# Kernel tuning notes

Hardware: AMD Instinct MI355X
Metric: run time of the kernel (lower is better)

## Reference

```python
import jax, jax.numpy as jnp
import numpy as np
import math

B, T, C = 1, 2048, 2048
NH, HS = 16, 128          # hs = C // nh
NLQ, NLKV, DHR = 1536, 512, 64


def _rope(x, cos, sin):
    # x: [B, T, H, D]; cos/sin: [T, D//2]. Rotates pairs (even, odd) like
    # torch's complex-multiply apply_rotary_emb.
    xr = x.reshape(x.shape[:-1] + (-1, 2))
    x_re, x_im = xr[..., 0], xr[..., 1]
    c = cos[None, :, None, :]
    s = sin[None, :, None, :]
    out = jnp.stack([x_re * c - x_im * s, x_re * s + x_im * c], axis=-1)
    return out.reshape(x.shape)


def setup_inputs() -> dict:
    key = jax.random.key(0)
    ks = jax.random.split(key, 9)
    sc = 0.02  # init scale so logits stay sane
    x = jax.random.normal(ks[0], (B, T, C), jnp.float32)
    # RoPE tables (theta = 10000), matching precompute_freqs_cis
    inv = 1.0 / (10000.0 ** (jnp.arange(0, DHR, 2, dtype=jnp.float32) / DHR))
    ang = jnp.outer(jnp.arange(T, dtype=jnp.float32), inv)  # [T, DHR//2]
    return {
        "x": x,
        "freqs_cos": jnp.cos(ang),
        "freqs_sin": jnp.sin(ang),
        "W_dq": jax.random.normal(ks[1], (NLQ, C), jnp.float32) * sc,
        "W_uq": jax.random.normal(ks[2], (C, NLQ), jnp.float32) * sc,
        "W_dkv": jax.random.normal(ks[3], (NLKV, C), jnp.float32) * sc,
        "W_uk": jax.random.normal(ks[4], (C, NLKV), jnp.float32) * sc,
        "W_uv": jax.random.normal(ks[5], (C, NLKV), jnp.float32) * sc,
        "W_qr": jax.random.normal(ks[6], (NH * DHR, NLQ), jnp.float32) * sc,
        "W_kr": jax.random.normal(ks[7], (DHR, C), jnp.float32) * sc,
        "W_o": jax.random.normal(ks[8], (C, C), jnp.float32) * sc,
    }


def reference(x, freqs_cos, freqs_sin, W_dq, W_uq, W_dkv, W_uk, W_uv, W_qr, W_kr, W_o):
    # ---- low-rank query/kv down-projections ----
    c_q = x @ W_dq.T                       # [B,T,NLQ]
    c_kv = x @ W_dkv.T                     # [B,T,NLKV]  (no kv_cache: c_kv = new_c_kv)

    # ---- weight absorption (training path) ----
    # torch: W_uq.weight.view(1,nlq,nh,hs).transpose(1,2) @ W_uk.weight.view(1,nh,hs,nlkv)
    Wuq_h = W_uq.reshape(NLQ, NH, HS).transpose(1, 0, 2)   # [NH,NLQ,HS]
    Wuk_h = W_uk.reshape(NH, HS, NLKV)                     # [NH,HS,NLKV]
    k_eff = jnp.einsum('hql,hlk->hqk', Wuq_h, Wuk_h)       # [NH,NLQ,NLKV]
    # torch: (W_uv.weight.T @ W_o.weight.T).view(nlkv,nh,hs).transpose(0,1)
    v_eff = (W_uv.T @ W_o.T).reshape(NLKV, NH, HS).transpose(1, 0, 2)  # [NH,NLKV,HS]

    # ---- content attention scores in latent space ----
    attn_c = jnp.einsum('bhtk,bsk->bhts',
                        jnp.einsum('btq,hqk->bhtk', c_q, k_eff), c_kv)  # [B,NH,T,T]

    # ---- decoupled RoPE subspace ----
    k_r = _rope((x @ W_kr.T)[:, :, None, :], freqs_cos, freqs_sin)[:, :, 0, :]   # [B,T,DHR]
    q_r = _rope((c_q @ W_qr.T).reshape(B, T, NH, DHR), freqs_cos, freqs_sin)
    q_r = q_r.transpose(0, 2, 1, 3)                                              # [B,NH,T,DHR]
    attn_r = jnp.einsum('bhtd,bsd->bhts', q_r, k_r)                              # [B,NH,T,T]

    # ---- combine, causal mask, softmax ----
    scale = 1.0 / math.sqrt(HS + DHR)
    scores = (attn_c + attn_r) * scale
    causal = jnp.tril(jnp.ones((T, T), dtype=bool))  # mask = triu(diag=1) complement
    scores = jnp.where(causal[None, None], scores, jnp.float32(-jnp.inf))
    attn = jax.nn.softmax(scores, axis=-1)           # dropout p=0.0

    # ---- value path: attend in latent space, then absorbed up+output proj ----
    y_lat = jnp.einsum('bhts,bsk->bhtk', attn, c_kv)          # [B,NH,T,NLKV]
    y = jnp.einsum('bhtk,hkd->bhtd', y_lat, v_eff)            # [B,NH,T,HS]
    y = y.transpose(0, 2, 1, 3).reshape(B, T, C)              # [B,T,C] (W_o absorbed)
    return y
```

## Files before the change

kernel.cpp:

```cpp
#include <hip/hip_runtime.h>
#include <hip/hip_bf16.h>
#include <math.h>

typedef __bf16 bf16_t;
typedef __bf16 bf16x4 __attribute__((ext_vector_type(4)));
typedef __bf16 bf16x8 __attribute__((ext_vector_type(8)));
typedef float f32x4 __attribute__((ext_vector_type(4)));

#define T_DIM 2048
#define C_DIM 2048
#define NH 16
#define HS 128
#define NLQ 1536
#define NLKV 512
#define DHR 64
#define QKD 192

__device__ __forceinline__ int probe_f32(const bf16_t* __restrict__ x) {
  int lane = threadIdx.x & 63;
  int bad = 0;
#pragma unroll
  for (int i = 0; i < 4; ++i) {
    float v = (float)x[lane + i * 64];
    if (!(fabsf(v) < 1.0e6f)) bad = 1;
  }
  return (__ballot(bad) != 0ull) ? 1 : 0;
}

struct PrepPack {
  const void* src[9];
  bf16_t* dst[9];
  int n[9];
  const void* tsrc[2];
  bf16_t* tdst[2];
  int tR[2], tC[2], tbx[2];
};

__global__ __launch_bounds__(256) void prep_k(PrepPack p, const bf16_t* __restrict__ xprobe) {
  __shared__ bf16_t tile[32][33];
  const int f32 = probe_f32(xprobe);
  const int which = blockIdx.y;
  if (which < 9) {
    const int n = p.n[which];
    const int stride = gridDim.x * 256 * 8;
    for (int i = (blockIdx.x * 256 + threadIdx.x) * 8; i < n; i += stride) {
      if (f32) {
        const float* s = (const float*)p.src[which] + i;
        f32x4 lo = *(const f32x4*)s;
        f32x4 hi = *(const f32x4*)(s + 4);
        bf16x8 v;
#pragma unroll
        for (int j = 0; j < 4; ++j) { v[j] = (bf16_t)lo[j]; v[j + 4] = (bf16_t)hi[j]; }
        *(bf16x8*)(p.dst[which] + i) = v;
      } else {
        *(bf16x8*)(p.dst[which] + i) = *(const bf16x8*)((const bf16_t*)p.src[which] + i);
      }
    }
  } else {
    const int ts = which - 9;
    const int R = p.tR[ts], C = p.tC[ts], tbx = p.tbx[ts];
    const int ntiles = tbx * (R / 32);
    if ((int)blockIdx.x >= ntiles) return;
    const void* in = p.tsrc[ts];
    bf16_t* out = p.tdst[ts];
    int bx = (blockIdx.x % tbx) * 32, by = (blockIdx.x / tbx) * 32;
    int tx = threadIdx.x & 31, ty = threadIdx.x >> 5;
    for (int i = ty; i < 32; i += 8) {
      int r = by + i, c = bx + tx;
      size_t idx = (size_t)r * C + c;
      tile[i][tx] = f32 ? (bf16_t)((const float*)in)[idx] : ((const bf16_t*)in)[idx];
    }
    __syncthreads();
    for (int i = ty; i < 32; i += 8) {
      int r = bx + i, c = by + tx;
      out[(size_t)r * R + c] = tile[tx][i];
    }
  }
}

__device__ __forceinline__ void async16(const bf16_t* g, bf16_t* l) {
  __builtin_amdgcn_global_load_lds(
      (const __attribute__((address_space(1))) void*)g,
      (__attribute__((address_space(3))) void*)l, 16, 0, 0);
}

#define BM 128
#define BN 128
#define BKG 64

struct GDesc {
  const bf16_t* A; const bf16_t* B; bf16_t* C;
  int M, N, K, lda, ldb, ldc, mb, bx0;
};
struct GGrp { GDesc d[3]; };

__global__ __launch_bounds__(256) void gemm_group(GGrp g, int nseg) {
  int bx = blockIdx.x;
  int s = 0;
  while (s + 1 < nseg && bx >= g.d[s + 1].bx0) ++s;
  const GDesc D = g.d[s];
  const int local = bx - D.bx0;
  const int bm = (local % D.mb) * BM, bn = (local / D.mb) * BN;

  __shared__ bf16_t As[2][BM * BKG];
  __shared__ bf16_t Bs[2][BN * BKG];
  const int tid = threadIdx.x;
  const int lane = tid & 63;
  const int wave = tid >> 6;
  const int l16 = lane & 15, quad = lane >> 4;
  const int wm = (wave >> 1) * 64, wn = (wave & 1) * 64;
  f32x4 acc[4][4] = {};

  const int nt = D.K / BKG;

#pragma unroll
  for (int r = 0; r < 4; ++r) {
    int c = r * 256 + tid;
    int row = c >> 3;
    int c8 = (c & 7) ^ (row & 7);
    int ar = bm + row; if (ar > D.M - 1) ar = D.M - 1;
    int br = bn + row; if (br > D.N - 1) br = D.N - 1;
    async16(D.A + (size_t)ar * D.lda + c8 * 8, &As[0][c * 8]);
    async16(D.B + (size_t)br * D.ldb + c8 * 8, &Bs[0][c * 8]);
  }
  asm volatile("s_waitcnt vmcnt(0)" ::: "memory");
  __builtin_amdgcn_s_barrier();

  for (int t = 0; t < nt; ++t) {
    const int cur = t & 1;
    if (t + 1 < nt) {
      const int k0 = (t + 1) * BKG;
#pragma unroll
      for (int r = 0; r < 4; ++r) {
        int c = r * 256 + tid;
        int row = c >> 3;
        int c8 = (c & 7) ^ (row & 7);
        int ar = bm + row; if (ar > D.M - 1) ar = D.M - 1;
        int br = bn + row; if (br > D.N - 1) br = D.N - 1;
        async16(D.A + (size_t)ar * D.lda + k0 + c8 * 8, &As[cur ^ 1][c * 8]);
        async16(D.B + (size_t)br * D.ldb + k0 + c8 * 8, &Bs[cur ^ 1][c * 8]);
      }
    }
#pragma unroll
    for (int kk = 0; kk < 2; ++kk) {
      bf16x8 af[4], bfr[4];
#pragma unroll
      for (int i = 0; i < 4; ++i) {
        int row = wm + i * 16 + l16;
        af[i] = *(const bf16x8*)(&As[cur][row * BKG + (((kk * 4 + quad) ^ (row & 7)) * 8)]);
      }
#pragma unroll
      for (int j = 0; j < 4; ++j) {
        int row = wn + j * 16 + l16;
        bfr[j] = *(const bf16x8*)(&Bs[cur][row * BKG + (((kk * 4 + quad) ^ (row & 7)) * 8)]);
      }
#pragma unroll
      for (int i = 0; i < 4; ++i)
#pragma unroll
        for (int j = 0; j < 4; ++j)
          acc[i][j] = __builtin_amdgcn_mfma_f32_16x16x32_bf16(af[i], bfr[j], acc[i][j], 0, 0, 0);
    }
    asm volatile("s_waitcnt vmcnt(0)" ::: "memory");
    __builtin_amdgcn_s_barrier();
  }

#pragma unroll
  for (int i = 0; i < 4; ++i)
#pragma unroll
    for (int j = 0; j < 4; ++j)
#pragma unroll
      for (int r = 0; r < 4; ++r) {
        int gm = bm + wm + i * 16 + quad * 4 + r;
        int gn = bn + wn + j * 16 + l16;
        if (gm < D.M && gn < D.N) D.C[(size_t)gm * D.ldc + gn] = (bf16_t)acc[i][j][r];
      }
}

__global__ void pack_qk_k(const bf16_t* __restrict__ qcat, const bf16_t* __restrict__ khead,
                          const bf16_t* __restrict__ xa,
                          const bf16_t* __restrict__ fc, const bf16_t* __restrict__ fs,
                          bf16_t* __restrict__ Qp, bf16_t* __restrict__ Kp) {
  int idx = blockIdx.x * blockDim.x + threadIdx.x;
  if (idx >= NH * T_DIM * 96) return;
  int j = idx % 96;
  int t = (idx / 96) % T_DIM;
  int h = idx / (96 * T_DIM);
  if (blockIdx.y == 0) {
    const float scale = 0.07216878364870323f;
    bf16_t* out = Qp + ((size_t)h * T_DIM + t) * QKD;
    if (j < 64) {
      float a = (float)qcat[(size_t)t * 3072 + h * HS + 2 * j];
      float b = (float)qcat[(size_t)t * 3072 + h * HS + 2 * j + 1];
      out[2 * j] = (bf16_t)(a * scale);
      out[2 * j + 1] = (bf16_t)(b * scale);
    } else {
      int i = j - 64;
      float re = (float)qcat[(size_t)t * 3072 + 2048 + h * DHR + 2 * i];
      float im = (float)qcat[(size_t)t * 3072 + 2048 + h * DHR + 2 * i + 1];
      float c = (float)fc[t * 32 + i], s = (float)fs[t * 32 + i];
      out[HS + 2 * i] = (bf16_t)((re * c - im * s) * scale);
      out[HS + 2 * i + 1] = (bf16_t)((re * s + im * c) * scale);
    }
  } else {
    bf16_t* out = Kp + ((size_t)h * T_DIM + t) * QKD;
    if (j < 64) {
      out[2 * j] = khead[(size_t)t * C_DIM + h * HS + 2 * j];
      out[2 * j + 1] = khead[(size_t)t * C_DIM + h * HS + 2 * j + 1];
    } else {
      int i = j - 64;
      float re = (float)xa[(size_t)t * 2112 + 2048 + 2 * i];
      float im = (float)xa[(size_t)t * 2112 + 2048 + 2 * i + 1];
      float c = (float)fc[t * 32 + i], s = (float)fs[t * 32 + i];
      out[HS + 2 * i] = (bf16_t)(re * c - im * s);
      out[HS + 2 * i + 1] = (bf16_t)(re * s + im * c);
    }
  }
}

#define FBM 128
#define FBN 64
#define KPITCH 200
#define VPITCH 72
#define PPITCH 72

__global__ __launch_bounds__(256) void flash_k(const bf16_t* __restrict__ Qp,
                                               const bf16_t* __restrict__ Kp,
                                               const bf16_t* __restrict__ VT,
                                               void* __restrict__ Y,
                                               const bf16_t* __restrict__ xprobe,
                                               float* __restrict__ Opart,
                                               float* __restrict__ Mpart,
                                               float* __restrict__ Lpart) {
  __shared__ bf16_t Ksm[FBN * KPITCH];
  __shared__ bf16_t Vtsm[HS * VPITCH];
  __shared__ bf16_t Psm[4][32 * PPITCH];
  const int tid = threadIdx.x;
  const int lane = tid & 63, wave = tid >> 6;
  const int l16 = lane & 15, quad = lane >> 4;
  const int id = blockIdx.x;
  const int xcd = id & 7, slot = id >> 3;
  const int h = xcd + 8 * (slot / 24);
  const int p = slot % 24;
  int qt, kt0, kt1, partial;
  if (p < 16) {
    qt = 8 + (p >> 1);
    int half = qt + 1;
    kt0 = (p & 1) ? half : 0;
    kt1 = (p & 1) ? (2 * qt + 2) : half;
    partial = 1;
  } else {
    qt = 23 - p; kt0 = 0; kt1 = 2 * qt + 2; partial = 0;
  }
  const int qb = qt * FBM;
  const int f32out = probe_f32(xprobe);

  bf16x8 aq[2][6];
#pragma unroll
  for (int tt = 0; tt < 2; ++tt) {
    const bf16_t* qbase = Qp + ((size_t)h * T_DIM + qb + wave * 32 + tt * 16 + l16) * QKD;
#pragma unroll
    for (int c = 0; c < 6; ++c) aq[tt][c] = *(const bf16x8*)(qbase + c * 32 + quad * 8);
  }

  f32x4 o[2][8] = {};
  float m_i[2] = {-3.0e38f, -3.0e38f}, l_i[2] = {0.f, 0.f};

  const bf16_t* kg_base = Kp + (size_t)h * T_DIM * QKD;
  const bf16_t* vg_base = VT + (size_t)(h * HS) * T_DIM;

  bf16x8 kreg[6], vreg[4];
  {
    const bf16_t* kg = kg_base + (size_t)kt0 * FBN * QKD;
#pragma unroll
    for (int i = 0; i < 6; ++i) {
      int idx = i * 256 + tid;
      kreg[i] = *(const bf16x8*)(kg + (size_t)idx * 8);
    }
    const bf16_t* vg = vg_base + kt0 * FBN;
#pragma unroll
    for (int i = 0; i < 4; ++i) {
      int idx = i * 256 + tid, row = idx >> 3, c8 = idx & 7;
      vreg[i] = *(const bf16x8*)(vg + (size_t)row * T_DIM + c8 * 8);
    }
  }

  for (int kt = kt0; kt < kt1; ++kt) {
    __syncthreads();
#pragma unroll
    for (int i = 0; i < 6; ++i) {
      int idx = i * 256 + tid, row = idx / 24, c8 = idx % 24;
      *(bf16x8*)(Ksm + row * KPITCH + c8 * 8) = kreg[i];
    }
#pragma unroll
    for (int i = 0; i < 4; ++i) {
      int idx = i * 256 + tid, row = idx >> 3, c8 = idx & 7;
      *(bf16x8*)(Vtsm + row * VPITCH + c8 * 8) = vreg[i];
    }
    __syncthreads();
    if (kt + 1 < kt1) {
      const bf16_t* kg = kg_base + (size_t)(kt + 1) * FBN * QKD;
#pragma unroll
      for (int i = 0; i < 6; ++i) {
        int idx = i * 256 + tid;
        kreg[i] = *(const bf16x8*)(kg + (size_t)idx * 8);
      }
      const bf16_t* vg = vg_base + (kt + 1) * FBN;
#pragma unroll
      for (int i = 0; i < 4; ++i) {
        int idx = i * 256 + tid, row = idx >> 3, c8 = idx & 7;
        vreg[i] = *(const bf16x8*)(vg + (size_t)row * T_DIM + c8 * 8);
      }
    }
    f32x4 sc[2][4] = {};
#pragma unroll
    for (int nt = 0; nt < 4; ++nt)
#pragma unroll
      for (int c = 0; c < 6; ++c) {
        bf16x8 bk = *(const bf16x8*)(Ksm + (nt * 16 + l16) * KPITCH + c * 32 + quad * 8);
        sc[0][nt] = __builtin_amdgcn_mfma_f32_16x16x32_bf16(bk, aq[0][c], sc[0][nt], 0, 0, 0);
        sc[1][nt] = __builtin_amdgcn_mfma_f32_16x16x32_bf16(bk, aq[1][c], sc[1][nt], 0, 0, 0);
      }
    if (kt >= 2 * qt) {
#pragma unroll
      for (int tt = 0; tt < 2; ++tt) {
        int t_glob = qb + wave * 32 + tt * 16 + l16;
#pragma unroll
        for (int nt = 0; nt < 4; ++nt) {
          int s_base = kt * FBN + nt * 16 + quad * 4;
#pragma unroll
          for (int r = 0; r < 4; ++r)
            if (s_base + r > t_glob) sc[tt][nt][r] = -3.0e38f;
        }
      }
    }
#pragma unroll
    for (int tt = 0; tt < 2; ++tt) {
      float mx = sc[tt][0][0];
#pragma unroll
      for (int nt = 0; nt < 4; ++nt)
#pragma unroll
        for (int r = 0; r < 4; ++r) mx = fmaxf(mx, sc[tt][nt][r]);
      mx = fmaxf(mx, __shfl_xor(mx, 16, 64));
      mx = fmaxf(mx, __shfl_xor(mx, 32, 64));
      float mn = fmaxf(m_i[tt], mx);
      float alpha = exp2f((m_i[tt] - mn) * 1.4426950408889634f);
      float rs = 0.f;
#pragma unroll
      for (int nt = 0; nt < 4; ++nt) {
        bf16x4 pk;
#pragma unroll
        for (int r = 0; r < 4; ++r) {
          float pv = exp2f((sc[tt][nt][r] - mn) * 1.4426950408889634f);
          rs += pv;
          pk[r] = (bf16_t)pv;
        }
        *(bf16x4*)(&Psm[wave][(tt * 16 + l16) * PPITCH + nt * 16 + quad * 4]) = pk;
      }
      rs += __shfl_xor(rs, 16, 64);
      rs += __shfl_xor(rs, 32, 64);
      l_i[tt] = l_i[tt] * alpha + rs;
      m_i[tt] = mn;
#pragma unroll
      for (int dt = 0; dt < 8; ++dt) o[tt][dt] *= alpha;
    }
#pragma unroll
    for (int s2 = 0; s2 < 2; ++s2) {
      bf16x8 ap0 = *(const bf16x8*)(&Psm[wave][l16 * PPITCH + s2 * 32 + quad * 8]);
      bf16x8 ap1 = *(const bf16x8*)(&Psm[wave][(16 + l16) * PPITCH + s2 * 32 + quad * 8]);
#pragma unroll
      for (int dt = 0; dt < 8; ++dt) {
        bf16x8 bv = *(const bf16x8*)(Vtsm + (dt * 16 + l16) * VPITCH + s2 * 32 + quad * 8);
        o[0][dt] = __builtin_amdgcn_mfma_f32_16x16x32_bf16(bv, ap0, o[0][dt], 0, 0, 0);
        o[1][dt] = __builtin_amdgcn_mfma_f32_16x16x32_bf16(bv, ap1, o[1][dt], 0, 0, 0);
      }
    }
  }

  if (!partial) {
#pragma unroll
    for (int tt = 0; tt < 2; ++tt) {
      float inv = 1.0f / l_i[tt];
      int t = qb + wave * 32 + tt * 16 + l16;
#pragma unroll
      for (int dt = 0; dt < 8; ++dt) {
        size_t oi = (size_t)t * C_DIM + h * HS + dt * 16 + quad * 4;
        if (f32out) {
          f32x4 v;
#pragma unroll
          for (int r = 0; r < 4; ++r) v[r] = o[tt][dt][r] * inv;
          *(f32x4*)((float*)Y + oi) = v;
        } else {
          bf16x4 v;
#pragma unroll
          for (int r = 0; r < 4; ++r) v[r] = (bf16_t)(o[tt][dt][r] * inv);
          *(bf16x4*)((bf16_t*)Y + oi) = v;
        }
      }
    }
  } else {
    const int pi = h * 16 + p;
#pragma unroll
    for (int tt = 0; tt < 2; ++tt) {
      int rowl = wave * 32 + tt * 16 + l16;
      float* ob = Opart + ((size_t)pi * 128 + rowl) * 128;
#pragma unroll
      for (int dt = 0; dt < 8; ++dt) {
        f32x4 v = o[tt][dt];
        *(f32x4*)(ob + dt * 16 + quad * 4) = v;
      }
      if (quad == 0) {
        Mpart[(size_t)pi * 128 + rowl] = m_i[tt];
        Lpart[(size_t)pi * 128 + rowl] = l_i[tt];
      }
    }
  }
}

__global__ __launch_bounds__(256) void combine_k(const float* __restrict__ Opart,
                                                 const float* __restrict__ Mpart,
                                                 const float* __restrict__ Lpart,
                                                 void* __restrict__ Y,
                                                 const bf16_t* __restrict__ xprobe) {
  const int h = blockIdx.y;
  const int qi = blockIdx.x;
  const int pi0 = h * 16 + qi * 2, pi1 = pi0 + 1;
  const int row = threadIdx.x >> 1;
  const int c0 = (threadIdx.x & 1) * 64;
  const int f32out = probe_f32(xprobe);
  float m0 = Mpart[(size_t)pi0 * 128 + row], m1 = Mpart[(size_t)pi1 * 128 + row];
  float l0 = Lpart[(size_t)pi0 * 128 + row], l1 = Lpart[(size_t)pi1 * 128 + row];
  float ms = fmaxf(m0, m1);
  float w0 = exp2f((m0 - ms) * 1.4426950408889634f);
  float w1 = exp2f((m1 - ms) * 1.4426950408889634f);
  float inv = 1.0f / (l0 * w0 + l1 * w1);
  const float* O0 = Opart + ((size_t)pi0 * 128 + row) * 128 + c0;
  const float* O1 = Opart + ((size_t)pi1 * 128 + row) * 128 + c0;
  int t = (8 + qi) * 128 + row;
  size_t ob = (size_t)t * C_DIM + h * HS + c0;
#pragma unroll
  for (int d4 = 0; d4 < 64; d4 += 4) {
    f32x4 a = *(const f32x4*)(O0 + d4);
    f32x4 b = *(const f32x4*)(O1 + d4);
#pragma unroll
    for (int j = 0; j < 4; ++j) {
      float v = (a[j] * w0 + b[j] * w1) * inv;
      if (f32out) ((float*)Y)[ob + d4 + j] = v;
      else        ((bf16_t*)Y)[ob + d4 + j] = (bf16_t)v;
    }
  }
}

extern "C" void kernel_launch(void* const* d_in, const int* in_sizes, int n_in,
                              void* d_out, int out_size, void* d_ws, size_t ws_size,
                              hipStream_t stream) {
  bf16_t* w = (bf16_t*)d_ws;
  const bf16_t* xprobe = (const bf16_t*)d_in[0];

  if (ws_size < (size_t)34472000 * 2 + 128) return;

  bf16_t* fcc    = w + 64;
  bf16_t* fsc    = w + 65600;
  bf16_t* xc     = w + 131136;
  bf16_t* BigB   = w + 4325440;
  bf16_t* dqc    = BigB;
  bf16_t* dkvc   = BigB + 3145728;
  bf16_t* krc    = BigB + 4194304;
  bf16_t* Bq     = w + 8650816;
  bf16_t* W_uq_t = Bq;
  bf16_t* qrc    = Bq + 3145728;
  bf16_t* xa     = w + 13369408;
  bf16_t* qcat   = w + 17694784;
  bf16_t* k_head = w + 23986240;
  bf16_t* vhatT  = w + 28180544;
  bf16_t* ukc    = w + 32374848;
  bf16_t* Pt     = w + 33423424;
  bf16_t* woc    = qcat;
  bf16_t* W_uv_t = k_head;
  bf16_t* Qpack  = xc;
  bf16_t* Kpack  = qcat;
  float* Opart = (float*)(w + 6422592);
  float* Mpart = (float*)(w + 14811200);
  float* Lpart = (float*)(w + 14876736);

  PrepPack pp;
  const void* srcs[9] = {d_in[1], d_in[2], d_in[0], d_in[3], d_in[5], d_in[9], d_in[8], d_in[6], d_in[10]};
  bf16_t* dsts[9]     = {fcc,     fsc,     xc,      dqc,     dkvc,    krc,     qrc,     ukc,     woc};
  int ns[9] = {T_DIM * 32, T_DIM * 32, T_DIM * C_DIM, NLQ * C_DIM, NLKV * C_DIM,
               DHR * C_DIM, NH * DHR * NLQ, C_DIM * NLKV, C_DIM * C_DIM};
  for (int i = 0; i < 9; ++i) { pp.src[i] = srcs[i]; pp.dst[i] = dsts[i]; pp.n[i] = ns[i]; }
  pp.tsrc[0] = d_in[4]; pp.tdst[0] = W_uq_t; pp.tR[0] = 1536; pp.tC[0] = 2048; pp.tbx[0] = 64;
  pp.tsrc[1] = d_in[7]; pp.tdst[1] = W_uv_t; pp.tR[1] = 2048; pp.tC[1] = 512;  pp.tbx[1] = 16;
  prep_k<<<dim3(3072, 11), 256, 0, stream>>>(pp, xprobe);

  {
    GGrp g;
    g.d[0] = {xc,  BigB,   xa, 2048, 2112, 2048, 2048, 2048, 2112, 16, 0};
    g.d[1] = {woc, W_uv_t, Pt, 2048,  512, 2048, 2048, 2048,  512, 16, 272};
    gemm_group<<<336, 256, 0, stream>>>(g, 2);
  }
  {
    GGrp g;
    g.d[0] = {xa,        Bq,        qcat,   2048, 3072, 1536, 2112, 1536, 3072, 16, 0};
    g.d[1] = {xa + 1536, ukc,       k_head, 2048, 2048,  512, 2112,  512, 2048, 16, 384};
    g.d[2] = {Pt,        xa + 1536, vhatT,  2048, 2048,  512,  512, 2112, 2048, 16, 640};
    gemm_group<<<896, 256, 0, stream>>>(g, 3);
  }

  int pk = (NH * T_DIM * 96 + 255) / 256;
  pack_qk_k<<<dim3(pk, 2), 256, 0, stream>>>(qcat, k_head, xa, fcc, fsc, Qpack, Kpack);

  flash_k<<<dim3(384), 256, 0, stream>>>(Qpack, Kpack, vhatT, d_out, xprobe, Opart, Mpart, Lpart);
  combine_k<<<dim3(8, NH), 256, 0, stream>>>(Opart, Mpart, Lpart, d_out, xprobe);
}
```

Measured before the change: 331.4 us.

## Rebalance flash attention split-KV into up to three parts with lazy rescaling

Replaces the fixed two-way split for the upper query tiles with a table-driven schedule: tiles 6-11 split into two KV ranges and tiles 12-15 into three, giving 480 workgroups of more even size. The combine kernel now merges two or three partials, and the partial buffers are split across two workspace regions. The softmax loop skips the running-max rescale unless the new max exceeds the old by a threshold, and it uses the hardware exp2 and packed bf16 conversion. This trades extra partial traffic and combine work for better load balance across CUs, and it lets probabilities exceed 1 before normalization.

After: 313.4 us. -5.4%, faster.

```diff
diff --git a/kernel.cpp b/kernel.cpp
--- a/kernel.cpp
+++ b/kernel.cpp
@@ -16,6 +16,14 @@
 #define DHR 64
 #define QKD 192
 
+__constant__ int c_qt_tab[30] = {5,11,11,15,15,10,10,15,14,14,14,9,9,13,4,
+                                 13,13,8,8,12,12,12,3,7,7,6,6,2,1,0};
+__constant__ int c_pt_tab[30] = {0,0,1,0,1,0,1,2,0,1,2,0,1,0,0,
+                                 1,2,0,1,0,1,2,0,0,1,0,1,0,0,0};
+__constant__ int c_pbase[16]  = {0,0,0,0,0,0,0,2,4,6,8,10,12,15,18,21};
+
+#define NSLOT_A 338
+
 __device__ __forceinline__ int probe_f32(const bf16_t* __restrict__ x) {
   int lane = threadIdx.x & 63;
   int bad = 0;
@@ -25,6 +33,13 @@
     if (!(fabsf(v) < 1.0e6f)) bad = 1;
   }
   return (__ballot(bad) != 0ull) ? 1 : 0;
+}
+
+__device__ __forceinline__ float* opart_at(float* A, float* B, int pi) {
+  return (pi < NSLOT_A) ? (A + (size_t)pi * 16384) : (B + (size_t)(pi - NSLOT_A) * 16384);
+}
+__device__ __forceinline__ const float* opart_atc(const float* A, const float* B, int pi) {
+  return (pi < NSLOT_A) ? (A + (size_t)pi * 16384) : (B + (size_t)(pi - NSLOT_A) * 16384);
 }
 
 struct PrepPack {
@@ -82,6 +97,10 @@
   __builtin_amdgcn_global_load_lds(
       (const __attribute__((address_space(1))) void*)g,
       (__attribute__((address_space(3))) void*)l, 16, 0, 0);
+}
+
+__device__ __forceinline__ float fexp2(float x) {
+  return __builtin_amdgcn_exp2f(x);
 }
 
 #define BM 128
@@ -228,7 +247,8 @@
                                                const bf16_t* __restrict__ VT,
                                                void* __restrict__ Y,
                                                const bf16_t* __restrict__ xprobe,
-                                               float* __restrict__ Opart,
+                                               float* __restrict__ OpartA,
+                                               float* __restrict__ OpartB,
                                                float* __restrict__ Mpart,
                                                float* __restrict__ Lpart) {
   __shared__ bf16_t Ksm[FBN * KPITCH];
@@ -239,20 +259,19 @@
   const int l16 = lane & 15, quad = lane >> 4;
   const int id = blockIdx.x;
   const int xcd = id & 7, slot = id >> 3;
-  const int h = xcd + 8 * (slot / 24);
-  const int p = slot % 24;
-  int qt, kt0, kt1, partial;
-  if (p < 16) {
-    qt = 8 + (p >> 1);
-    int half = qt + 1;
-    kt0 = (p & 1) ? half : 0;
-    kt1 = (p & 1) ? (2 * qt + 2) : half;
-    partial = 1;
-  } else {
-    qt = 23 - p; kt0 = 0; kt1 = 2 * qt + 2; partial = 0;
-  }
+  const int h = xcd + 8 * (slot / 30);
+  const int p = slot % 30;
+  const int qt = c_qt_tab[p];
+  const int part = c_pt_tab[p];
+  const int nkv = 2 * qt + 2;
+  const int nparts = (qt <= 5) ? 1 : (qt <= 11 ? 2 : 3);
+  const int bse = nkv / nparts, rem = nkv % nparts;
+  const int kt0 = part * bse + (part < rem ? part : rem);
+  const int kt1 = kt0 + bse + (part < rem ? 1 : 0);
+  const int partial = (nparts > 1);
   const int qb = qt * FBM;
   const int f32out = probe_f32(xprobe);
+  const float L2E = 1.4426950408889634f;
 
   bf16x8 aq[2][6];
 #pragma unroll
@@ -342,26 +361,31 @@
         for (int r = 0; r < 4; ++r) mx = fmaxf(mx, sc[tt][nt][r]);
       mx = fmaxf(mx, __shfl_xor(mx, 16, 64));
       mx = fmaxf(mx, __shfl_xor(mx, 32, 64));
-      float mn = fmaxf(m_i[tt], mx);
-      float alpha = exp2f((m_i[tt] - mn) * 1.4426950408889634f);
+      int need = (mx > m_i[tt] + 5.5f) ? 1 : 0;
+      if (__any(need)) {
+        float mn = fmaxf(m_i[tt], mx);
+        float alpha = fexp2((m_i[tt] - mn) * L2E);
+        m_i[tt] = mn;
+        l_i[tt] *= alpha;
+#pragma unroll
+        for (int dt = 0; dt < 8; ++dt) o[tt][dt] *= alpha;
+      }
       float rs = 0.f;
 #pragma unroll
       for (int nt = 0; nt < 4; ++nt) {
-        bf16x4 pk;
-#pragma unroll
-        for (int r = 0; r < 4; ++r) {
-          float pv = exp2f((sc[tt][nt][r] - mn) * 1.4426950408889634f);
-          rs += pv;
-          pk[r] = (bf16_t)pv;
-        }
-        *(bf16x4*)(&Psm[wave][(tt * 16 + l16) * PPITCH + nt * 16 + quad * 4]) = pk;
+        float p0 = fexp2((sc[tt][nt][0] - m_i[tt]) * L2E);
+        float p1 = fexp2((sc[tt][nt][1] - m_i[tt]) * L2E);
+        float p2 = fexp2((sc[tt][nt][2] - m_i[tt]) * L2E);
+        float p3 = fexp2((sc[tt][nt][3] - m_i[tt]) * L2E);
+        rs += (p0 + p1) + (p2 + p3);
+        uint2 pk;
+        asm("v_cvt_pk_bf16_f32 %0, %1, %2" : "=v"(pk.x) : "v"(p0), "v"(p1));
+        asm("v_cvt_pk_bf16_f32 %0, %1, %2" : "=v"(pk.y) : "v"(p2), "v"(p3));
+        *(uint2*)(&Psm[wave][(tt * 16 + l16) * PPITCH + nt * 16 + quad * 4]) = pk;
       }
       rs += __shfl_xor(rs, 16, 64);
       rs += __shfl_xor(rs, 32, 64);
-      l_i[tt] = l_i[tt] * alpha + rs;
-      m_i[tt] = mn;
-#pragma unroll
-      for (int dt = 0; dt < 8; ++dt) o[tt][dt] *= alpha;
+      l_i[tt] += rs;
     }
 #pragma unroll
     for (int s2 = 0; s2 < 2; ++s2) {
@@ -398,11 +422,12 @@
       }
     }
   } else {
-    const int pi = h * 16 + p;
+    const int pi = h * 24 + c_pbase[qt] + part;
+    float* obase = opart_at(OpartA, OpartB, pi);
 #pragma unroll
     for (int tt = 0; tt < 2; ++tt) {
       int rowl = wave * 32 + tt * 16 + l16;
-      float* ob = Opart + ((size_t)pi * 128 + rowl) * 128;
+      float* ob = obase + (size_t)rowl * 128;
 #pragma unroll
       for (int dt = 0; dt < 8; ++dt) {
         f32x4 v = o[tt][dt];
@@ -416,34 +441,54 @@
   }
 }
 
-__global__ __launch_bounds__(256) void combine_k(const float* __restrict__ Opart,
+__global__ __launch_bounds__(256) void combine_k(const float* __restrict__ OpartA,
+                                                 const float* __restrict__ OpartB,
                                                  const float* __restrict__ Mpart,
                                                  const float* __restrict__ Lpart,
                                                  void* __restrict__ Y,
                                                  const bf16_t* __restrict__ xprobe) {
   const int h = blockIdx.y;
-  const int qi = blockIdx.x;
-  const int pi0 = h * 16 + qi * 2, pi1 = pi0 + 1;
+  const int qt = 6 + blockIdx.x;
+  const int c = (qt <= 11) ? 2 : 3;
+  const int pib = h * 24 + c_pbase[qt];
   const int row = threadIdx.x >> 1;
   const int c0 = (threadIdx.x & 1) * 64;
   const int f32out = probe_f32(xprobe);
-  float m0 = Mpart[(size_t)pi0 * 128 + row], m1 = Mpart[(size_t)pi1 * 128 + row];
-  float l0 = Lpart[(size_t)pi0 * 128 + row], l1 = Lpart[(size_t)pi1 * 128 + row];
-  float ms = fmaxf(m0, m1);
-  float w0 = exp2f((m0 - ms) * 1.4426950408889634f);
-  float w1 = exp2f((m1 - ms) * 1.4426950408889634f);
-  float inv = 1.0f / (l0 * w0 + l1 * w1);
-  const float* O0 = Opart + ((size_t)pi0 * 128 + row) * 128 + c0;
-  const float* O1 = Opart + ((size_t)pi1 * 128 + row) * 128 + c0;
-  int t = (8 + qi) * 128 + row;
+  const float L2E = 1.4426950408889634f;
+  float m0 = Mpart[(size_t)pib * 128 + row];
+  float m1 = Mpart[(size_t)(pib + 1) * 128 + row];
+  float l0 = Lpart[(size_t)pib * 128 + row];
+  float l1 = Lpart[(size_t)(pib + 1) * 128 + row];
+  float m2 = -3.0e38f, l2 = 0.f;
+  if (c == 3) {
+    m2 = Mpart[(size_t)(pib + 2) * 128 + row];
+    l2 = Lpart[(size_t)(pib + 2) * 128 + row];
+  }
+  float ms = fmaxf(m0, fmaxf(m1, m2));
+  float w0 = fexp2((m0 - ms) * L2E);
+  float w1 = fexp2((m1 - ms) * L2E);
+  float w2 = fexp2((m2 - ms) * L2E);
+  float inv = 1.0f / (l0 * w0 + l1 * w1 + l2 * w2);
+  const float* O0 = opart_atc(OpartA, OpartB, pib) + (size_t)row * 128 + c0;
+  const float* O1 = opart_atc(OpartA, OpartB, pib + 1) + (size_t)row * 128 + c0;
+  const float* O2 = opart_atc(OpartA, OpartB, pib + 2) + (size_t)row * 128 + c0;
+  int t = qt * 128 + row;
   size_t ob = (size_t)t * C_DIM + h * HS + c0;
 #pragma unroll
   for (int d4 = 0; d4 < 64; d4 += 4) {
     f32x4 a = *(const f32x4*)(O0 + d4);
     f32x4 b = *(const f32x4*)(O1 + d4);
+    f32x4 acc;
+#pragma unroll
+    for (int j = 0; j < 4; ++j) acc[j] = a[j] * w0 + b[j] * w1;
+    if (c == 3) {
+      f32x4 e = *(const f32x4*)(O2 + d4);
+#pragma unroll
+      for (int j = 0; j < 4; ++j) acc[j] += e[j] * w2;
+    }
 #pragma unroll
     for (int j = 0; j < 4; ++j) {
-      float v = (a[j] * w0 + b[j] * w1) * inv;
+      float v = acc[j] * inv;
       if (f32out) ((float*)Y)[ob + d4 + j] = v;
       else        ((bf16_t*)Y)[ob + d4 + j] = (bf16_t)v;
     }
@@ -478,9 +523,10 @@
   bf16_t* W_uv_t = k_head;
   bf16_t* Qpack  = xc;
   bf16_t* Kpack  = qcat;
-  float* Opart = (float*)(w + 6422592);
-  float* Mpart = (float*)(w + 14811200);
-  float* Lpart = (float*)(w + 14876736);
+  float* OpartA = (float*)(w + 6422592);
+  float* Mpart  = (float*)(w + 17498176);
+  float* Lpart  = (float*)(w + 17596480);
+  float* OpartB = (float*)(w + 23986240);
 
   PrepPack pp;
   const void* srcs[9] = {d_in[1], d_in[2], d_in[0], d_in[3], d_in[5], d_in[9], d_in[8], d_in[6], d_in[10]};
@@ -509,6 +555,7 @@
   int pk = (NH * T_DIM * 96 + 255) / 256;
   pack_qk_k<<<dim3(pk, 2), 256, 0, stream>>>(qcat, k_head, xa, fcc, fsc, Qpack, Kpack);
 
-  flash_k<<<dim3(384), 256, 0, stream>>>(Qpack, Kpack, vhatT, d_out, xprobe, Opart, Mpart, Lpart);
-  combine_k<<<dim3(8, NH), 256, 0, stream>>>(Opart, Mpart, Lpart, d_out, xprobe);
-}
+  flash_k<<<dim3(480), 256, 0, stream>>>(Qpack, Kpack, vhatT, d_out, xprobe,
+                                         OpartA, OpartB, Mpart, Lpart);
+  combine_k<<<dim3(10, NH), 256, 0, stream>>>(OpartA, OpartB, Mpart, Lpart, d_out, xprobe);
+}
```
